# Kernel tuning notes

Hardware: AMD Instinct MI355X
Metric: run time of the kernel (lower is better)

## Reference

```python
import jax, jax.numpy as jnp
import numpy as np
from jax import lax

EPS = 1e-20
BN_EPS = 1e-5
ATTN_SCALE = 2.8284271247461903  # sqrt(d_l=8)
NS = (32, 32, 32, 10)
DS = (8, 8, 8, 16)


def squash(x):
    # Efficient-CapsNet squash: (1 - 1/(exp(||x||)+eps)) * x/(||x||+eps)
    norm = jnp.linalg.norm(x, axis=-1, keepdims=True)
    return (1.0 - 1.0 / (jnp.exp(norm) + EPS)) * (x / (norm + EPS))


def conv2d(x, w, b, stride, groups=1):
    y = lax.conv_general_dilated(
        x, w, window_strides=(stride, stride), padding='VALID',
        dimension_numbers=('NCHW', 'OIHW', 'NCHW'),
        feature_group_count=groups)
    return y + b[None, :, None, None]


def bn(x, g, b, m, v):
    inv = g / jnp.sqrt(v + BN_EPS)
    return x * inv[None, :, None, None] + (b - m * inv)[None, :, None, None]


def fccaps(U_l, W):
    # U_l: (b, n_l, d_l), W: (n_l, n_h, d_l, d_h)
    U_hat = jnp.einsum('bij,ikjl->bikl', U_l, W)          # (b, n_l, n_h, d_h)
    A = jnp.einsum('bikl,bhkl->bhik', U_hat, U_hat)        # (b, n_l, n_l, n_h)
    A_sum = jnp.sum(A, axis=-2)                            # (b, n_l, n_h)
    C = jax.nn.softmax(A_sum / ATTN_SCALE, axis=-1)        # (b, n_l, n_h)
    U_h = jnp.einsum('bikl,bik->bkl', U_hat, C)            # (b, n_h, d_h)
    return squash(U_h)


def setup_inputs() -> dict:
    key = jax.random.key(0)
    ks = jax.random.split(key, 8)
    B = 512
    x = jax.random.normal(ks[0], (B, 1, 39, 39), dtype=jnp.float32)
    conv1_w = jax.random.normal(ks[1], (128, 1, 3, 3), jnp.float32) * 0.2
    conv1_b = jnp.zeros((128,), jnp.float32)
    conv2_w = jax.random.normal(ks[2], (256, 128, 3, 3), jnp.float32) * 0.04
    conv2_b = jnp.zeros((256,), jnp.float32)
    conv3_w = jax.random.normal(ks[3], (256, 1, 9, 9), jnp.float32) * 0.1  # depthwise
    conv3_b = jnp.zeros((256,), jnp.float32)
    bn1_g = jnp.ones((128,), jnp.float32); bn1_b = jnp.zeros((128,), jnp.float32)
    bn1_m = jnp.zeros((128,), jnp.float32); bn1_v = jnp.ones((128,), jnp.float32)
    bn2_g = jnp.ones((256,), jnp.float32); bn2_b = jnp.zeros((256,), jnp.float32)
    bn2_m = jnp.zeros((256,), jnp.float32); bn2_v = jnp.ones((256,), jnp.float32)
    # capsule weights, kaiming-ish scale sqrt(2/fan_in) with fan_in = n_h*d_l*d_h
    def caps_w(k, n_l, n_h, d_l, d_h):
        std = np.sqrt(2.0 / (n_h * d_l * d_h))
        return jax.random.normal(k, (n_l, n_h, d_l, d_h), jnp.float32) * std
    W1 = caps_w(ks[4], NS[0], NS[1], DS[0], DS[1])
    W2 = caps_w(ks[5], NS[1], NS[2], DS[1], DS[2])
    W3 = caps_w(ks[6], NS[2], NS[3], DS[2], DS[3])
    return dict(x=x, conv1_w=conv1_w, conv1_b=conv1_b,
                bn1_g=bn1_g, bn1_b=bn1_b, bn1_m=bn1_m, bn1_v=bn1_v,
                conv2_w=conv2_w, conv2_b=conv2_b,
                bn2_g=bn2_g, bn2_b=bn2_b, bn2_m=bn2_m, bn2_v=bn2_v,
                conv3_w=conv3_w, conv3_b=conv3_b, W1=W1, W2=W2, W3=W3)


def reference(x, conv1_w, conv1_b, bn1_g, bn1_b, bn1_m, bn1_v,
              conv2_w, conv2_b, bn2_g, bn2_b, bn2_m, bn2_v,
              conv3_w, conv3_b, W1, W2, W3):
    h = jax.nn.relu(bn(conv2d(x, conv1_w, conv1_b, 2), bn1_g, bn1_b, bn1_m, bn1_v))
    h = jax.nn.relu(bn(conv2d(h, conv2_w, conv2_b, 2), bn2_g, bn2_b, bn2_m, bn2_v))
    h = conv2d(h, conv3_w, conv3_b, 1, groups=256)        # (B, 256, 1, 1)
    u = h.reshape(h.shape[0], NS[0], DS[0])                # (B, 32, 8)
    u = squash(u)
    for W in (W1, W2, W3):
        u = fccaps(u, W)
    return u  # (B, 10, 16)
```

## Files before the change

### kernel.cpp

```cpp
#include <hip/hip_runtime.h>


typedef __attribute__((ext_vector_type(8))) short short8;
typedef __attribute__((ext_vector_type(4))) float f32x4;

__device__ __forceinline__ ushort f2bf(float x) {
    uint u = __float_as_uint(x);
    return (ushort)((u + 0x7FFFu + ((u >> 16) & 1u)) >> 16);
}
__device__ __forceinline__ void bfsplit(float x, ushort& h, ushort& l) {
    h = f2bf(x);
    float hf = __uint_as_float(((uint)h) << 16);
    l = f2bf(x - hf);
}

__global__ __launch_bounds__(256) void k_prep(
    const float* __restrict__ w2, uint* __restrict__ Bt,
    const float* __restrict__ w3, float* __restrict__ w3T,
    const float* __restrict__ W1, const float* __restrict__ W2,
    const float* __restrict__ W3, float* __restrict__ Wr1,
    float* __restrict__ Wr2, float* __restrict__ Wr3) {
    __shared__ __align__(16) float wbuf[64 * 288];
    const int b = blockIdx.x, t = threadIdx.x;
    if (b < 144) {
        const int sidx = b >> 2, coq = b & 3;
        const int chunk = sidx / 9, tap = sidx - chunk * 9;
        const int co0 = coq * 64;
        for (int idx = t; idx < 4608; idx += 256) {
            const int n = idx / 72, q = idx - n * 72;
            ((float4*)wbuf)[n * 72 + q] =
                *(const float4*)(w2 + (size_t)(co0 + n) * 1152 + chunk * 288 + q * 4);
        }
        __syncthreads();
        const int n = t & 63, dg = (t >> 6) * 4;
        const int cot = coq >> 1, nn = ((coq & 1) * 64) + n;
        uint* dst = Bt + (size_t)(sidx * 2 + cot) * 4096;
#pragma unroll
        for (int dd = 0; dd < 4; ++dd) {
            const int d = dg + dd;
            const float x = wbuf[n * 288 + (2 * d) * 9 + tap];
            const float y = wbuf[n * 288 + (2 * d + 1) * 9 + tap];
            ushort xh, xl, yh, yl;
            bfsplit(x, xh, xl);
            bfsplit(y, yh, yl);
            dst[nn * 16 + d]        = (uint)xh | ((uint)yh << 16);
            dst[2048 + nn * 16 + d] = (uint)xl | ((uint)yl << 16);
        }
    } else if (b < 225) {
        const int p = b - 144;
        w3T[p * 256 + t] = w3[t * 81 + p];
    } else {
        const int bb = b - 225;
        const int layer = bb >> 5, blk = bb & 31;
        const float* src = layer == 0 ? W1 : (layer == 1 ? W2 : W3);
        float* dst = layer == 0 ? Wr1 : (layer == 1 ? Wr2 : Wr3);
        const int d_h = (layer == 2) ? 16 : 8;
        const int total = (layer == 2) ? 5120 : 8192;
        for (int idx = blk * 256 + t; idx < 8 * total; idx += 32 * 256) {
            const int j = idx / total, e = idx - j * total;
            const int ik = e / d_h, l = e - ik * d_h;
            dst[idx] = src[(ik * 8 + j) * d_h + l];
        }
    }
}

__global__ __launch_bounds__(256, 2) void k_conv1(
    const float* __restrict__ x, const float* __restrict__ w,
    const float* __restrict__ bias, const float* __restrict__ g,
    const float* __restrict__ bb, const float* __restrict__ bm,
    const float* __restrict__ bv, ushort* __restrict__ h1) {
    __shared__ __align__(16) float xs[1521];
    __shared__ float wls[1152];
    __shared__ float2 scsh[128];
    __shared__ __align__(16) uint stage[11552];
    const int b = blockIdx.x, t = threadIdx.x;
    const float* xb = x + (size_t)b * 1521;
    for (int i = t; i < 1521; i += 256) xs[i] = xb[i];
    for (int i = t; i < 1152; i += 256) wls[i] = w[i];
    if (t < 128) {
        const float inv = g[t] * rsqrtf(bv[t] + 1e-5f);
        scsh[t] = make_float2(inv, bias[t] * inv + bb[t] - bm[t] * inv);
    }
    const int ol = t >> 6, pg = t & 63;
    ushort* stg = (ushort*)stage;
    __syncthreads();
    for (int chunk = 0; chunk < 4; ++chunk) {
        float wr[8][9];
        float2 ss[8];
#pragma unroll
        for (int j = 0; j < 8; ++j) {
            const int c = chunk * 32 + ol * 8 + j;
#pragma unroll
            for (int k = 0; k < 9; ++k) wr[j][k] = wls[c * 9 + k];
            ss[j] = scsh[c];
        }
        for (int p = pg; p < 361; p += 64) {
            const int y = p / 19, xq = p - y * 19;
            const int base = y * 78 + xq * 2;
            const float x0 = xs[base],      x1 = xs[base + 1],  x2 = xs[base + 2];
            const float x3 = xs[base + 39], x4 = xs[base + 40], x5 = xs[base + 41];
            const float x6 = xs[base + 78], x7 = xs[base + 79], x8 = xs[base + 80];
            short8 hs, ls;
#pragma unroll
            for (int j = 0; j < 8; ++j) {
                const float acc = x0 * wr[j][0] + x1 * wr[j][1] + x2 * wr[j][2] +
                                  x3 * wr[j][3] + x4 * wr[j][4] + x5 * wr[j][5] +
                                  x6 * wr[j][6] + x7 * wr[j][7] + x8 * wr[j][8];
                const float v = fmaxf(fmaf(acc, ss[j].x, ss[j].y), 0.0f);
                ushort hh, lw;
                bfsplit(v, hh, lw);
                hs[j] = (short)hh;
                ls[j] = (short)lw;
            }
            if ((xq & 1) == 0) {
                const int pos = y * 10 + (xq >> 1);
                *(short8*)(stg + ol * 1520 + pos * 8)         = hs;
                *(short8*)(stg + 11552 + ol * 1520 + pos * 8) = ls;
            } else {
                const int pos = y * 9 + (xq >> 1);
                *(short8*)(stg + 6080 + ol * 1368 + pos * 8)  = hs;
                *(short8*)(stg + 17632 + ol * 1368 + pos * 8) = ls;
            }
        }
        __syncthreads();
        {
            uint4* dst = (uint4*)(h1 + (size_t)b * 92416 + chunk * 23104);
            const uint4* src = (const uint4*)stage;
#pragma unroll
            for (int k = 0; k < 11; ++k) dst[t + k * 256] = src[t + k * 256];
            if (t < 72) dst[t + 11 * 256] = src[t + 11 * 256];
        }
        __syncthreads();
    }
}

__global__ __launch_bounds__(256, 3) void k_conv2(
    const uint* __restrict__ h1u, const uint* __restrict__ Bt,
    const float* __restrict__ g,
    const float* __restrict__ bb, const float* __restrict__ bm,
    const float* __restrict__ bv, const float* __restrict__ bias,
    const float* __restrict__ w3T, float* __restrict__ Uws) {
    __shared__ __align__(16) uint raw[11552];
    __shared__ float ured[128];
    const int t = threadIdx.x;
    const int lane = t & 63, wave = t >> 6;
    const int ln15 = lane & 15, lq = lane >> 4;
    const int wm = (wave >> 1) * 48, wn = (wave & 1) * 64;
    const int gg = blockIdx.x;
    const int bi  = ((gg >> 4) << 3) | (gg & 7);
    const int cot = (gg >> 3) & 1;
    const int co0 = cot * 128;

    int PE[3], PO[3];
#pragma unroll
    for (int i = 0; i < 3; ++i) {
        const int m = wm + i * 16 + ln15;
        const int p = m < 81 ? m : 80;
        const int oh = p / 9, ow = p - oh * 9;
        PE[i] = lq * 760 + oh * 80 + ow * 4;
        PO[i] = 3040 + lq * 684 + oh * 72 + ow * 4;
    }
    int BRDg[4];
#pragma unroll
    for (int j = 0; j < 4; ++j) {
        const int n = wn + j * 16 + ln15;
        BRDg[j] = n * 16 + lq * 4;
    }

    f32x4 acc[3][4] = {};
    uint4 Bn[8];
    {
        const uint* bp = Bt + (size_t)cot * 4096;
#pragma unroll
        for (int j = 0; j < 4; ++j) {
            Bn[j]     = *(const uint4*)(bp + BRDg[j]);
            Bn[4 + j] = *(const uint4*)(bp + 2048 + BRDg[j]);
        }
    }

#pragma unroll
    for (int c = 0; c < 4; ++c) {
        __syncthreads();
        {
            const uint4* src = (const uint4*)(h1u + (size_t)(bi * 4 + c) * 11552);
            uint4* dst = (uint4*)raw;
            uint4 tmp[11];
#pragma unroll
            for (int k = 0; k < 11; ++k) tmp[k] = src[t + k * 256];
            const bool extra = (t < 72);
            uint4 te;
            if (extra) te = src[t + 11 * 256];
#pragma unroll
            for (int k = 0; k < 11; ++k) dst[t + k * 256] = tmp[k];
            if (extra) dst[t + 11 * 256] = te;
        }
        __syncthreads();
        short8 a_h[3];
#pragma unroll
        for (int i = 0; i < 3; ++i)
            a_h[i] = *reinterpret_cast<const short8*>(raw + PE[i]);
#pragma unroll
        for (int tap = 0; tap < 9; ++tap) {
            const int s = c * 9 + tap;
            uint4 Bc[8];
#pragma unroll
            for (int q = 0; q < 8; ++q) Bc[q] = Bn[q];
            if (s < 35) {
                const uint* bp = Bt + (size_t)((s + 1) * 2 + cot) * 4096;
#pragma unroll
                for (int j = 0; j < 4; ++j) {
                    Bn[j]     = *(const uint4*)(bp + BRDg[j]);
                    Bn[4 + j] = *(const uint4*)(bp + 2048 + BRDg[j]);
                }
            }
            const int kh = tap / 3, kw = tap - kh * 3;
            const int odd = kw & 1;
            const int sE = kh * 40 + (kw >> 1) * 4;
            const int sO = kh * 36;
            short8 a_l[3];
#pragma unroll
            for (int i = 0; i < 3; ++i) {
                const int addr = odd ? (PO[i] + sO) : (PE[i] + sE);
                a_l[i] = *reinterpret_cast<const short8*>(raw + addr + 5776);
            }
            short8 a_hn[3];
            if (tap < 8) {
                const int tap2 = tap + 1;
                const int kh2 = tap2 / 3, kw2 = tap2 - kh2 * 3;
                const int odd2 = kw2 & 1;
                const int sE2 = kh2 * 40 + (kw2 >> 1) * 4;
                const int sO2 = kh2 * 36;
#pragma unroll
                for (int i = 0; i < 3; ++i) {
                    const int addr2 = odd2 ? (PO[i] + sO2) : (PE[i] + sE2);
                    a_hn[i] = *reinterpret_cast<const short8*>(raw + addr2);
                }
            }
            short8 bh[4], bl[4];
#pragma unroll
            for (int j = 0; j < 4; ++j) {
                bh[j] = __builtin_bit_cast(short8, Bc[j]);
                bl[j] = __builtin_bit_cast(short8, Bc[4 + j]);
            }
#pragma unroll
            for (int i = 0; i < 3; ++i)
#pragma unroll
                for (int j = 0; j < 4; ++j)
                    acc[i][j] = __builtin_amdgcn_mfma_f32_16x16x32_bf16(a_h[i], bh[j], acc[i][j], 0, 0, 0);
#pragma unroll
            for (int i = 0; i < 3; ++i)
#pragma unroll
                for (int j = 0; j < 4; ++j)
                    acc[i][j] = __builtin_amdgcn_mfma_f32_16x16x32_bf16(a_h[i], bl[j], acc[i][j], 0, 0, 0);
#pragma unroll
            for (int i = 0; i < 3; ++i)
#pragma unroll
                for (int j = 0; j < 4; ++j)
                    acc[i][j] = __builtin_amdgcn_mfma_f32_16x16x32_bf16(a_l[i], bh[j], acc[i][j], 0, 0, 0);
            if (tap < 8) {
#pragma unroll
                for (int i = 0; i < 3; ++i) a_h[i] = a_hn[i];
            }
        }
    }

    float scj[4], shj[4];
#pragma unroll
    for (int j = 0; j < 4; ++j) {
        const int co = co0 + wn + j * 16 + ln15;
        const float inv = g[co] * rsqrtf(bv[co] + 1e-5f);
        scj[j] = inv;
        shj[j] = bias[co] * inv + bb[co] - bm[co] * inv;
    }
    float usum[4] = {0.f, 0.f, 0.f, 0.f};
#pragma unroll
    for (int i = 0; i < 3; ++i)
#pragma unroll
        for (int r = 0; r < 4; ++r) {
            const int m = wm + i * 16 + lq * 4 + r;
            if (m < 81) {
                const float* wrow = w3T + m * 256 + co0;
#pragma unroll
                for (int j = 0; j < 4; ++j) {
                    const int col = wn + j * 16 + ln15;
                    const float v = fmaxf(fmaf(acc[i][j][r], scj[j], shj[j]), 0.0f);
                    usum[j] = fmaf(v, wrow[col], usum[j]);
                }
            }
        }
#pragma unroll
    for (int j = 0; j < 4; ++j) {
        usum[j] += __shfl_xor(usum[j], 16);
        usum[j] += __shfl_xor(usum[j], 32);
    }
    if (lq == 0 && wm == 0) {
#pragma unroll
        for (int j = 0; j < 4; ++j) ured[(wn >> 6) * 64 + j * 16 + ln15] = usum[j];
    }
    __syncthreads();
    if (lq == 0 && wm == 48) {
#pragma unroll
        for (int j = 0; j < 4; ++j) {
            const int col = wn + j * 16 + ln15;
            Uws[(size_t)bi * 256 + co0 + col] =
                usum[j] + ured[(wn >> 6) * 64 + j * 16 + ln15];
        }
    }
}

__device__ __forceinline__ void fccaps_block(
    const int n_l, const int n_h, const int d_h, const float* __restrict__ Wr,
    float* U, float* Uh, float* Sv, float* Av, float* Cv, float* coefs,
    float* outU, const int t) {
    const int nkd = n_h * d_h;
    const int total = n_l * nkd;
    __syncthreads();
    for (int e = t; e < total; e += 256) {
        const int i = e / nkd;
        const float* up = U + i * 8;
        float acc = 0.0f;
#pragma unroll
        for (int j = 0; j < 8; ++j) acc += up[j] * Wr[j * total + e];
        Uh[e] = acc;
    }
    __syncthreads();
    for (int e = t; e < nkd; e += 256) {
        float acc = 0.0f;
        for (int i = 0; i < n_l; ++i) acc += Uh[i * nkd + e];
        Sv[e] = acc;
    }
    __syncthreads();
    for (int e = t; e < n_l * n_h; e += 256) {
        const int h = e / n_h, k = e - h * n_h;
        float acc = 0.0f;
        for (int l = 0; l < d_h; ++l)
            acc += Uh[h * nkd + k * d_h + l] * Sv[k * d_h + l];
        Av[e] = acc;
    }
    __syncthreads();
    {
        const int h = t >> 3, sub = t & 7;
        const float invs = 1.0f / 2.8284271247461903f;
        float mx = -1e30f;
        for (int k = sub; k < n_h; k += 8) mx = fmaxf(mx, Av[h * n_h + k]);
        mx = fmaxf(mx, __shfl_xor(mx, 1));
        mx = fmaxf(mx, __shfl_xor(mx, 2));
        mx = fmaxf(mx, __shfl_xor(mx, 4));
        float sum = 0.0f;
        for (int k = sub; k < n_h; k += 8) {
            const float ev = expf((Av[h * n_h + k] - mx) * invs);
            Cv[h * n_h + k] = ev;
            sum += ev;
        }
        sum += __shfl_xor(sum, 1);
        sum += __shfl_xor(sum, 2);
        sum += __shfl_xor(sum, 4);
        const float r = 1.0f / sum;
        for (int k = sub; k < n_h; k += 8) Cv[h * n_h + k] *= r;
    }
    __syncthreads();
    for (int e = t; e < nkd; e += 256) {
        const int k = e / d_h;
        float acc = 0.0f;
        for (int i = 0; i < n_l; ++i) acc += Uh[i * nkd + e] * Cv[i * n_h + k];
        Sv[e] = acc;
    }
    __syncthreads();
    if (t < n_h) {
        float ssq = 0.0f;
        for (int l = 0; l < d_h; ++l) { const float uv = Sv[t * d_h + l]; ssq += uv * uv; }
        const float n = sqrtf(ssq);
        coefs[t] = (1.0f - 1.0f / (expf(n) + 1e-20f)) / (n + 1e-20f);
    }
    __syncthreads();
    for (int e = t; e < nkd; e += 256) outU[e] = Sv[e] * coefs[e / d_h];
}

__global__ __launch_bounds__(256) void k_caps(
    const float* __restrict__ Uws, const float* __restrict__ b3,
    const float* __restrict__ Wr1, const float* __restrict__ Wr2,
    const float* __restrict__ Wr3, float* __restrict__ out) {
    __shared__ float U[256];
    __shared__ float Uh[8192];
    __shared__ float Sv[256];
    __shared__ float Av[1024];
    __shared__ float Cv[1024];
    __shared__ float coefs[32];
    const int b = blockIdx.x, t = threadIdx.x;
    U[t] = Uws[(size_t)b * 256 + t] + b3[t];
    __syncthreads();
    if (t < 32) {
        float ssq = 0.0f;
        for (int j = 0; j < 8; ++j) { const float uv = U[t * 8 + j]; ssq += uv * uv; }
        const float n = sqrtf(ssq);
        coefs[t] = (1.0f - 1.0f / (expf(n) + 1e-20f)) / (n + 1e-20f);
    }
    __syncthreads();
    U[t] *= coefs[t >> 3];
    fccaps_block(32, 32,  8, Wr1, U, Uh, Sv, Av, Cv, coefs, U, t);
    fccaps_block(32, 32,  8, Wr2, U, Uh, Sv, Av, Cv, coefs, U, t);
    fccaps_block(32, 10, 16, Wr3, U, Uh, Sv, Av, Cv, coefs, out + (size_t)b * 160, t);
}

extern "C" void kernel_launch(void* const* d_in, const int* in_sizes, int n_in,
                              void* d_out, int out_size, void* d_ws, size_t ws_size,
                              hipStream_t stream) {
    const float* x    = (const float*)d_in[0];
    const float* c1w  = (const float*)d_in[1];
    const float* c1b  = (const float*)d_in[2];
    const float* bn1g = (const float*)d_in[3];
    const float* bn1b = (const float*)d_in[4];
    const float* bn1m = (const float*)d_in[5];
    const float* bn1v = (const float*)d_in[6];
    const float* c2w  = (const float*)d_in[7];
    const float* c2b  = (const float*)d_in[8];
    const float* bn2g = (const float*)d_in[9];
    const float* bn2b = (const float*)d_in[10];
    const float* bn2m = (const float*)d_in[11];
    const float* bn2v = (const float*)d_in[12];
    const float* c3w  = (const float*)d_in[13];
    const float* c3b  = (const float*)d_in[14];
    const float* W1   = (const float*)d_in[15];
    const float* W2   = (const float*)d_in[16];
    const float* W3   = (const float*)d_in[17];
    float* out = (float*)d_out;
    uint*  wsu = (uint*)d_ws;
    float* wsf = (float*)d_ws;

    ushort* h1  = (ushort*)wsu;
    float*  Uws = wsf + 23658496;
    uint*   Bt  = wsu + 23789568;
    float*  w3T = wsf + 24084480;
    float*  Wr1 = wsf + 24105216;
    float*  Wr2 = wsf + 24170752;
    float*  Wr3 = wsf + 24236288;

    k_prep<<<dim3(321), 256, 0, stream>>>(c2w, Bt, c3w, w3T, W1, W2, W3,
                                          Wr1, Wr2, Wr3);
    k_conv1<<<dim3(512), 256, 0, stream>>>(x, c1w, c1b, bn1g, bn1b, bn1m, bn1v, h1);
    k_conv2<<<dim3(1024), 256, 0, stream>>>((const uint*)h1, Bt, bn2g, bn2b, bn2m, bn2v,
                                            c2b, w3T, Uws);
    k_caps<<<dim3(512), 256, 0, stream>>>(Uws, c3b, Wr1, Wr2, Wr3, out);
}
```

Baseline: 233.2 us.

## Retile conv2 waves to cover all rows and loop two jobs per block

Reassigns conv2's wave tiling so each wave covers all 96 (81 valid) output positions and 32 output channels, instead of a 48x64 quadrant. This removes the cross-wave LDS reduction and its extra barrier. The grid is halved to 512 blocks, each handling two (image, channel-half) jobs in sequence, and launch bounds drop from 3 to 2 blocks per CU. B-fragment register and global-load traffic per wave shrinks, but each wave now issues twice as many LDS A reads per tap and the A-load prefetch across taps is gone. The lower occupancy target and the serial jobs per block may expose more latency.

Result: slower. 459.9 us (+97.2%).

```diff
diff --git a/kernel.cpp b/kernel.cpp
--- a/kernel.cpp
+++ b/kernel.cpp
@@ -134,176 +134,150 @@
     }
 }
 
-__global__ __launch_bounds__(256, 3) void k_conv2(
+__global__ __launch_bounds__(256, 2) void k_conv2(
     const uint* __restrict__ h1u, const uint* __restrict__ Bt,
     const float* __restrict__ g,
     const float* __restrict__ bb, const float* __restrict__ bm,
     const float* __restrict__ bv, const float* __restrict__ bias,
     const float* __restrict__ w3T, float* __restrict__ Uws) {
     __shared__ __align__(16) uint raw[11552];
-    __shared__ float ured[128];
     const int t = threadIdx.x;
     const int lane = t & 63, wave = t >> 6;
     const int ln15 = lane & 15, lq = lane >> 4;
-    const int wm = (wave >> 1) * 48, wn = (wave & 1) * 64;
-    const int gg = blockIdx.x;
-    const int bi  = ((gg >> 4) << 3) | (gg & 7);
-    const int cot = (gg >> 3) & 1;
-    const int co0 = cot * 128;
-
-    int PE[3], PO[3];
-#pragma unroll
-    for (int i = 0; i < 3; ++i) {
-        const int m = wm + i * 16 + ln15;
+    const int wn = wave * 32;
+
+    int PE[6], PO[6];
+#pragma unroll
+    for (int i = 0; i < 6; ++i) {
+        const int m = i * 16 + ln15;
         const int p = m < 81 ? m : 80;
         const int oh = p / 9, ow = p - oh * 9;
         PE[i] = lq * 760 + oh * 80 + ow * 4;
         PO[i] = 3040 + lq * 684 + oh * 72 + ow * 4;
     }
-    int BRDg[4];
-#pragma unroll
-    for (int j = 0; j < 4; ++j) {
+    int BRDg[2];
+#pragma unroll
+    for (int j = 0; j < 2; ++j) {
         const int n = wn + j * 16 + ln15;
         BRDg[j] = n * 16 + lq * 4;
     }
 
-    f32x4 acc[3][4] = {};
-    uint4 Bn[8];
-    {
-        const uint* bp = Bt + (size_t)cot * 4096;
-#pragma unroll
-        for (int j = 0; j < 4; ++j) {
-            Bn[j]     = *(const uint4*)(bp + BRDg[j]);
-            Bn[4 + j] = *(const uint4*)(bp + 2048 + BRDg[j]);
-        }
-    }
-
-#pragma unroll
-    for (int c = 0; c < 4; ++c) {
-        __syncthreads();
+    for (int job = 0; job < 2; ++job) {
+        const int gg = blockIdx.x + job * 512;
+        const int bi  = ((gg >> 4) << 3) | (gg & 7);
+        const int cot = (gg >> 3) & 1;
+        const int co0 = cot * 128;
+
+        f32x4 acc[6][2] = {};
+        uint4 Bn[4];
         {
-            const uint4* src = (const uint4*)(h1u + (size_t)(bi * 4 + c) * 11552);
-            uint4* dst = (uint4*)raw;
-            uint4 tmp[11];
-#pragma unroll
-            for (int k = 0; k < 11; ++k) tmp[k] = src[t + k * 256];
-            const bool extra = (t < 72);
-            uint4 te;
-            if (extra) te = src[t + 11 * 256];
-#pragma unroll
-            for (int k = 0; k < 11; ++k) dst[t + k * 256] = tmp[k];
-            if (extra) dst[t + 11 * 256] = te;
-        }
-        __syncthreads();
-        short8 a_h[3];
-#pragma unroll
-        for (int i = 0; i < 3; ++i)
-            a_h[i] = *reinterpret_cast<const short8*>(raw + PE[i]);
-#pragma unroll
-        for (int tap = 0; tap < 9; ++tap) {
-            const int s = c * 9 + tap;
-            uint4 Bc[8];
-#pragma unroll
-            for (int q = 0; q < 8; ++q) Bc[q] = Bn[q];
-            if (s < 35) {
-                const uint* bp = Bt + (size_t)((s + 1) * 2 + cot) * 4096;
-#pragma unroll
-                for (int j = 0; j < 4; ++j) {
-                    Bn[j]     = *(const uint4*)(bp + BRDg[j]);
-                    Bn[4 + j] = *(const uint4*)(bp + 2048 + BRDg[j]);
+            const uint* bp = Bt + (size_t)cot * 4096;
+#pragma unroll
+            for (int j = 0; j < 2; ++j) {
+                Bn[j]     = *(const uint4*)(bp + BRDg[j]);
+                Bn[2 + j] = *(const uint4*)(bp + 2048 + BRDg[j]);
+            }
+        }
+
+#pragma unroll
+        for (int c = 0; c < 4; ++c) {
+            __syncthreads();
+            {
+                const uint4* src = (const uint4*)(h1u + (size_t)(bi * 4 + c) * 11552);
+                uint4* dst = (uint4*)raw;
+                uint4 tmp[11];
+#pragma unroll
+                for (int k = 0; k < 11; ++k) tmp[k] = src[t + k * 256];
+                const bool extra = (t < 72);
+                uint4 te;
+                if (extra) te = src[t + 11 * 256];
+#pragma unroll
+                for (int k = 0; k < 11; ++k) dst[t + k * 256] = tmp[k];
+                if (extra) dst[t + 11 * 256] = te;
+            }
+            __syncthreads();
+#pragma unroll
+            for (int tap = 0; tap < 9; ++tap) {
+                const int s = c * 9 + tap;
+                uint4 Bc[4];
+#pragma unroll
+                for (int q = 0; q < 4; ++q) Bc[q] = Bn[q];
+                if (s < 35) {
+                    const uint* bp = Bt + (size_t)((s + 1) * 2 + cot) * 4096;
+#pragma unroll
+                    for (int j = 0; j < 2; ++j) {
+                        Bn[j]     = *(const uint4*)(bp + BRDg[j]);
+                        Bn[2 + j] = *(const uint4*)(bp + 2048 + BRDg[j]);
+                    }
                 }
-            }
-            const int kh = tap / 3, kw = tap - kh * 3;
-            const int odd = kw & 1;
-            const int sE = kh * 40 + (kw >> 1) * 4;
-            const int sO = kh * 36;
-            short8 a_l[3];
-#pragma unroll
-            for (int i = 0; i < 3; ++i) {
-                const int addr = odd ? (PO[i] + sO) : (PE[i] + sE);
-                a_l[i] = *reinterpret_cast<const short8*>(raw + addr + 5776);
-            }
-            short8 a_hn[3];
-            if (tap < 8) {
-                const int tap2 = tap + 1;
-                const int kh2 = tap2 / 3, kw2 = tap2 - kh2 * 3;
-                const int odd2 = kw2 & 1;
-                const int sE2 = kh2 * 40 + (kw2 >> 1) * 4;
-                const int sO2 = kh2 * 36;
-#pragma unroll
-                for (int i = 0; i < 3; ++i) {
-                    const int addr2 = odd2 ? (PO[i] + sO2) : (PE[i] + sE2);
-                    a_hn[i] = *reinterpret_cast<const short8*>(raw + addr2);
+                const int kh = tap / 3, kw = tap - kh * 3;
+                const int odd = kw & 1;
+                const int sE = kh * 40 + (kw >> 1) * 4;
+                const int sO = kh * 36;
+                short8 a_h[6], a_l[6];
+#pragma unroll
+                for (int i = 0; i < 6; ++i) {
+                    const int addr = odd ? (PO[i] + sO) : (PE[i] + sE);
+                    a_h[i] = *reinterpret_cast<const short8*>(raw + addr);
+                    a_l[i] = *reinterpret_cast<const short8*>(raw + addr + 5776);
                 }
-            }
-            short8 bh[4], bl[4];
-#pragma unroll
-            for (int j = 0; j < 4; ++j) {
-                bh[j] = __builtin_bit_cast(short8, Bc[j]);
-                bl[j] = __builtin_bit_cast(short8, Bc[4 + j]);
-            }
-#pragma unroll
-            for (int i = 0; i < 3; ++i)
-#pragma unroll
-                for (int j = 0; j < 4; ++j)
-                    acc[i][j] = __builtin_amdgcn_mfma_f32_16x16x32_bf16(a_h[i], bh[j], acc[i][j], 0, 0, 0);
-#pragma unroll
-            for (int i = 0; i < 3; ++i)
-#pragma unroll
-                for (int j = 0; j < 4; ++j)
-                    acc[i][j] = __builtin_amdgcn_mfma_f32_16x16x32_bf16(a_h[i], bl[j], acc[i][j], 0, 0, 0);
-#pragma unroll
-            for (int i = 0; i < 3; ++i)
-#pragma unroll
-                for (int j = 0; j < 4; ++j)
-                    acc[i][j] = __builtin_amdgcn_mfma_f32_16x16x32_bf16(a_l[i], bh[j], acc[i][j], 0, 0, 0);
-            if (tap < 8) {
-#pragma unroll
-                for (int i = 0; i < 3; ++i) a_h[i] = a_hn[i];
-            }
-        }
-    }
-
-    float scj[4], shj[4];
-#pragma unroll
-    for (int j = 0; j < 4; ++j) {
-        const int co = co0 + wn + j * 16 + ln15;
-        const float inv = g[co] * rsqrtf(bv[co] + 1e-5f);
-        scj[j] = inv;
-        shj[j] = bias[co] * inv + bb[co] - bm[co] * inv;
-    }
-    float usum[4] = {0.f, 0.f, 0.f, 0.f};
-#pragma unroll
-    for (int i = 0; i < 3; ++i)
-#pragma unroll
-        for (int r = 0; r < 4; ++r) {
-            const int m = wm + i * 16 + lq * 4 + r;
-            if (m < 81) {
-                const float* wrow = w3T + m * 256 + co0;
-#pragma unroll
-                for (int j = 0; j < 4; ++j) {
-                    const int col = wn + j * 16 + ln15;
-                    const float v = fmaxf(fmaf(acc[i][j][r], scj[j], shj[j]), 0.0f);
-                    usum[j] = fmaf(v, wrow[col], usum[j]);
+                short8 bh[2], bl[2];
+#pragma unroll
+                for (int j = 0; j < 2; ++j) {
+                    bh[j] = __builtin_bit_cast(short8, Bc[j]);
+                    bl[j] = __builtin_bit_cast(short8, Bc[2 + j]);
                 }
-            }
-        }
-#pragma unroll
-    for (int j = 0; j < 4; ++j) {
-        usum[j] += __shfl_xor(usum[j], 16);
-        usum[j] += __shfl_xor(usum[j], 32);
-    }
-    if (lq == 0 && wm == 0) {
-#pragma unroll
-        for (int j = 0; j < 4; ++j) ured[(wn >> 6) * 64 + j * 16 + ln15] = usum[j];
-    }
-    __syncthreads();
-    if (lq == 0 && wm == 48) {
-#pragma unroll
-        for (int j = 0; j < 4; ++j) {
-            const int col = wn + j * 16 + ln15;
-            Uws[(size_t)bi * 256 + co0 + col] =
-                usum[j] + ured[(wn >> 6) * 64 + j * 16 + ln15];
+#pragma unroll
+                for (int i = 0; i < 6; ++i)
+#pragma unroll
+                    for (int j = 0; j < 2; ++j)
+                        acc[i][j] = __builtin_amdgcn_mfma_f32_16x16x32_bf16(a_h[i], bh[j], acc[i][j], 0, 0, 0);
+#pragma unroll
+                for (int i = 0; i < 6; ++i)
+#pragma unroll
+                    for (int j = 0; j < 2; ++j)
+                        acc[i][j] = __builtin_amdgcn_mfma_f32_16x16x32_bf16(a_h[i], bl[j], acc[i][j], 0, 0, 0);
+#pragma unroll
+                for (int i = 0; i < 6; ++i)
+#pragma unroll
+                    for (int j = 0; j < 2; ++j)
+                        acc[i][j] = __builtin_amdgcn_mfma_f32_16x16x32_bf16(a_l[i], bh[j], acc[i][j], 0, 0, 0);
+            }
+        }
+
+        float scj[2], shj[2];
+#pragma unroll
+        for (int j = 0; j < 2; ++j) {
+            const int co = co0 + wn + j * 16 + ln15;
+            const float inv = g[co] * rsqrtf(bv[co] + 1e-5f);
+            scj[j] = inv;
+            shj[j] = bias[co] * inv + bb[co] - bm[co] * inv;
+        }
+        float usum[2] = {0.f, 0.f};
+#pragma unroll
+        for (int i = 0; i < 6; ++i)
+#pragma unroll
+            for (int r = 0; r < 4; ++r) {
+                const int m = i * 16 + lq * 4 + r;
+                if (m < 81) {
+                    const float* wrow = w3T + m * 256 + co0;
+#pragma unroll
+                    for (int j = 0; j < 2; ++j) {
+                        const int col = wn + j * 16 + ln15;
+                        const float v = fmaxf(fmaf(acc[i][j][r], scj[j], shj[j]), 0.0f);
+                        usum[j] = fmaf(v, wrow[col], usum[j]);
+                    }
+                }
+            }
+#pragma unroll
+        for (int j = 0; j < 2; ++j) {
+            usum[j] += __shfl_xor(usum[j], 16);
+            usum[j] += __shfl_xor(usum[j], 32);
+        }
+        if (lq == 0) {
+#pragma unroll
+            for (int j = 0; j < 2; ++j)
+                Uws[(size_t)bi * 256 + co0 + wn + j * 16 + ln15] = usum[j];
         }
     }
 }
@@ -438,7 +412,7 @@
     k_prep<<<dim3(321), 256, 0, stream>>>(c2w, Bt, c3w, w3T, W1, W2, W3,
                                           Wr1, Wr2, Wr3);
     k_conv1<<<dim3(512), 256, 0, stream>>>(x, c1w, c1b, bn1g, bn1b, bn1m, bn1v, h1);
-    k_conv2<<<dim3(1024), 256, 0, stream>>>((const uint*)h1, Bt, bn2g, bn2b, bn2m, bn2v,
-                                            c2b, w3T, Uws);
+    k_conv2<<<dim3(512), 256, 0, stream>>>((const uint*)h1, Bt, bn2g, bn2b, bn2m, bn2v,
+                                           c2b, w3T, Uws);
     k_caps<<<dim3(512), 256, 0, stream>>>(Uws, c3b, Wr1, Wr2, Wr3, out);
 }
```
